# Performance work log

Hardware: AMD Instinct MI355X
Metric: run time of the kernel (lower is better)

The kernel has to match this reference:

```python
import jax, jax.numpy as jnp
import numpy as np

NEG_INF = -9e15
ALPHA = 0.2  # LeakyReLU negative slope

N = 4096
NFEAT = 512
NHID = 256
NEMBED = 128
NHEADS = 4
OUT1 = NHID // NHEADS   # 64
OUT2 = NEMBED // NHEADS # 32


def _gat_layer(x, adj_mask, W, a):
    # x: [N, F_in]; adj_mask: [N, N] bool; W: [H, F_in, F_out]; a: [H, 2*F_out]
    Fo = W.shape[-1]
    Wh = jnp.einsum('nf,hfo->hno', x, W)                     # [H, N, Fo]
    a_src = jnp.einsum('hno,ho->hn', Wh, a[:, :Fo])          # [H, N]
    a_dst = jnp.einsum('hno,ho->hn', Wh, a[:, Fo:])          # [H, N]
    e = a_src[:, :, None] + a_dst[:, None, :]                # [H, N, N]
    e = jax.nn.leaky_relu(e, negative_slope=ALPHA)
    e = jnp.where(adj_mask[None, :, :], e, NEG_INF)
    att = jax.nn.softmax(e, axis=-1)                         # [H, N, N]
    h = jnp.einsum('hnm,hmo->hno', att, Wh)                  # [H, N, Fo]
    h = jax.nn.elu(h)                                        # concat=True -> ELU
    # concat heads: [N, H*Fo]
    return jnp.transpose(h, (1, 0, 2)).reshape(x.shape[0], -1)


def setup_inputs() -> dict:
    key = jax.random.key(0)
    k1, k2, k3, k4, k5, k6 = jax.random.split(key, 6)
    x = jax.random.normal(k1, (N, NFEAT), dtype=jnp.float32)
    adj = (jax.random.uniform(k2, (N, N)) < 0.01).astype(jnp.float32)
    # per-head GAT params, xavier-uniform-like init (stacked over heads)
    def xavier(k, shape, fan):
        bound = np.sqrt(6.0 / fan)
        return jax.random.uniform(k, shape, minval=-bound, maxval=bound, dtype=jnp.float32)
    W1 = xavier(k3, (NHEADS, NFEAT, OUT1), NFEAT + OUT1)
    a1 = xavier(k4, (NHEADS, 2 * OUT1), 2 * OUT1 + 1)
    W2 = xavier(k5, (NHEADS, NHID, OUT2), NHID + OUT2)
    a2 = xavier(k6, (NHEADS, 2 * OUT2), 2 * OUT2 + 1)
    return {'x': x, 'adj': adj, 'W1': W1, 'a1': a1, 'W2': W2, 'a2': a2}


def reference(x, adj, W1, a1, W2, a2):
    # eval mode: dropout is identity
    adj_mask = adj > 0
    h1 = _gat_layer(x, adj_mask, W1, a1)    # [N, NHID]
    h2 = _gat_layer(h1, adj_mask, W2, a2)   # [N, NEMBED]
    return h2
```

## Files before the change

kernel.cpp:

```cpp
#include <hip/hip_runtime.h>
#include <hip/hip_bf16.h>
#include <cstdint>
#include <cstddef>

#define NNODES 4096
#define NHEADS 4
#define NBR_STRIDE 128

typedef __attribute__((ext_vector_type(8))) short bf16x8v;
typedef __attribute__((ext_vector_type(4))) float f32x4;

__device__ inline unsigned short bf16_rn(float f) {
    unsigned int u = __float_as_uint(f);
    u += 0x7FFFu + ((u >> 16) & 1u);
    return (unsigned short)(u >> 16);
}
__device__ inline float bf16_f32(unsigned short s) {
    return __uint_as_float(((unsigned int)s) << 16);
}

__device__ inline void build_nbr_body3(
    char* arena,
    const float* __restrict__ adj, int* __restrict__ nbr, int* __restrict__ deg,
    int row) {
    int* slots = (int*)arena;
    int* cnts  = (int*)(arena + 2048);
    int wave = threadIdx.x >> 6;
    int lane = threadIdx.x & 63;
    const float4* arow =
        reinterpret_cast<const float4*>(adj + (size_t)row * NNODES) + wave * 256;
    float4 v[4];
    #pragma unroll
    for (int it = 0; it < 4; ++it) v[it] = arow[it * 64 + lane];
    unsigned long long lt = (1ull << lane) - 1ull;
    int* slot = slots + wave * 128;
    int base = 0;
    #pragma unroll
    for (int it = 0; it < 4; ++it) {
        bool b0 = v[it].x > 0.f, b1 = v[it].y > 0.f, b2 = v[it].z > 0.f, b3 = v[it].w > 0.f;
        unsigned long long m0 = __ballot(b0);
        unsigned long long m1 = __ballot(b1);
        unsigned long long m2 = __ballot(b2);
        unsigned long long m3 = __ballot(b3);
        int pre = __popcll(m0 & lt) + __popcll(m1 & lt) +
                  __popcll(m2 & lt) + __popcll(m3 & lt);
        int pos = base + pre;
        int colb = wave * 1024 + it * 256 + lane * 4;
        if (b0) { if (pos < NBR_STRIDE) slot[pos] = colb;     pos++; }
        if (b1) { if (pos < NBR_STRIDE) slot[pos] = colb + 1; pos++; }
        if (b2) { if (pos < NBR_STRIDE) slot[pos] = colb + 2; pos++; }
        if (b3) { if (pos < NBR_STRIDE) slot[pos] = colb + 3; pos++; }
        base += __popcll(m0) + __popcll(m1) + __popcll(m2) + __popcll(m3);
    }
    if (lane == 0) cnts[wave] = base < NBR_STRIDE ? base : NBR_STRIDE;
    __syncthreads();
    int c0 = cnts[0], c1 = cnts[1], c2 = cnts[2];
    int tot = c0 + c1 + c2 + cnts[3];
    if (tot > NBR_STRIDE) tot = NBR_STRIDE;
    int t = threadIdx.x;
    if (t < tot) {
        int val;
        if (t < c0)                val = slots[t];
        else if (t < c0 + c1)      val = slots[128 + t - c0];
        else if (t < c0 + c1 + c2) val = slots[256 + t - c0 - c1];
        else                       val = slots[384 + t - c0 - c1 - c2];
        nbr[row * NBR_STRIDE + t] = val;
    }
    if (t == 0) deg[row] = tot;
}

__global__ __launch_bounds__(256) void pack_b_both_kernel(
    const float* __restrict__ W1, const float* __restrict__ W2,
    unsigned short* __restrict__ B1h, unsigned short* __restrict__ B1l,
    unsigned short* __restrict__ B2h, unsigned short* __restrict__ B2l) {
    int t = blockIdx.x * 256 + threadIdx.x;
    if (t < 256 * 512) {
        int n = t >> 9, k = t & 511;
        int h = n >> 6, o = n & 63;
        float v = W1[((size_t)h * 512 + k) * 64 + o];
        unsigned short hi = bf16_rn(v);
        B1h[t] = hi;
        B1l[t] = bf16_rn(v - bf16_f32(hi));
    } else {
        int u = t - 256 * 512;
        if (u < 128 * 256) {
            int n = u >> 8, k = u & 255;
            int h = n >> 5, o = n & 31;
            float v = W2[((size_t)h * 256 + k) * 32 + o];
            unsigned short hi = bf16_rn(v);
            B2h[u] = hi;
            B2l[u] = bf16_rn(v - bf16_f32(hi));
        }
    }
}

template <int K, int N, int FO, int BK, bool ASPLIT>
__device__ inline void gemm_body(
    char* arena,
    const float* __restrict__ A,
    const unsigned short* __restrict__ Ah, const unsigned short* __restrict__ Al,
    const unsigned short* __restrict__ Bh, const unsigned short* __restrict__ Bl,
    const float* __restrict__ a, float* __restrict__ C,
    float* __restrict__ asrc, float* __restrict__ adst,
    int bx, int by) {
    constexpr int BM = 32, BN = 64, LP = BK + 8;
    constexpr int ALD = BM * LP * 2;
    constexpr int BLD = BN * LP * 2;
    typedef unsigned short (*lds_t)[LP];
    lds_t Alh = (lds_t)(arena);
    lds_t All = (lds_t)(arena + ALD);
    lds_t Blh = (lds_t)(arena + 2 * ALD);
    lds_t Bll = (lds_t)(arena + 2 * ALD + BLD);
    float* reds = (float*)(arena + 2 * ALD + 2 * BLD);
    float* redd = (float*)(arena + 2 * ALD + 2 * BLD + 256);
    int tid = threadIdx.x;
    int wave = tid >> 6, lane = tid & 63;
    int rowBase = bx * BM;
    int colBase = by * BN;
    int wr = wave >> 1, wc = wave & 1;
    int lr = lane & 15, lk = lane >> 4;
    f32x4 acc0 = {0.f, 0.f, 0.f, 0.f};
    f32x4 acc1 = {0.f, 0.f, 0.f, 0.f};

    for (int k0 = 0; k0 < K; k0 += BK) {
        if constexpr (BK == 32) {
            int ar = tid >> 3, acf = (tid & 7) * 4;
            int br = tid >> 2, bc = (tid & 3) * 8;
            uint4 bh = *reinterpret_cast<const uint4*>(&Bh[(size_t)(colBase + br) * K + k0 + bc]);
            uint4 bl = *reinterpret_cast<const uint4*>(&Bl[(size_t)(colBase + br) * K + k0 + bc]);
            if constexpr (ASPLIT) {
                uint2 avh = *reinterpret_cast<const uint2*>(&Ah[(size_t)(rowBase + ar) * K + k0 + acf]);
                uint2 avl = *reinterpret_cast<const uint2*>(&Al[(size_t)(rowBase + ar) * K + k0 + acf]);
                __syncthreads();
                *reinterpret_cast<uint2*>(&Alh[ar][acf]) = avh;
                *reinterpret_cast<uint2*>(&All[ar][acf]) = avl;
                *reinterpret_cast<uint4*>(&Blh[br][bc]) = bh;
                *reinterpret_cast<uint4*>(&Bll[br][bc]) = bl;
            } else {
                float4 a0 = *reinterpret_cast<const float4*>(&A[(size_t)(rowBase + ar) * K + k0 + acf]);
                __syncthreads();
                ushort4 h4, l4;
                h4.x = bf16_rn(a0.x); l4.x = bf16_rn(a0.x - bf16_f32(h4.x));
                h4.y = bf16_rn(a0.y); l4.y = bf16_rn(a0.y - bf16_f32(h4.y));
                h4.z = bf16_rn(a0.z); l4.z = bf16_rn(a0.z - bf16_f32(h4.z));
                h4.w = bf16_rn(a0.w); l4.w = bf16_rn(a0.w - bf16_f32(h4.w));
                *reinterpret_cast<ushort4*>(&Alh[ar][acf]) = h4;
                *reinterpret_cast<ushort4*>(&All[ar][acf]) = l4;
                *reinterpret_cast<uint4*>(&Blh[br][bc]) = bh;
                *reinterpret_cast<uint4*>(&Bll[br][bc]) = bl;
            }
        } else {
            int ar = tid >> 3, ac = (tid & 7) * 8;
            uint4 bh0 = *reinterpret_cast<const uint4*>(&Bh[(size_t)(colBase + ar) * K + k0 + ac]);
            uint4 bl0 = *reinterpret_cast<const uint4*>(&Bl[(size_t)(colBase + ar) * K + k0 + ac]);
            uint4 bh1 = *reinterpret_cast<const uint4*>(&Bh[(size_t)(colBase + 32 + ar) * K + k0 + ac]);
            uint4 bl1 = *reinterpret_cast<const uint4*>(&Bl[(size_t)(colBase + 32 + ar) * K + k0 + ac]);
            if constexpr (ASPLIT) {
                uint4 avh = *reinterpret_cast<const uint4*>(&Ah[(size_t)(rowBase + ar) * K + k0 + ac]);
                uint4 avl = *reinterpret_cast<const uint4*>(&Al[(size_t)(rowBase + ar) * K + k0 + ac]);
                __syncthreads();
                *reinterpret_cast<uint4*>(&Alh[ar][ac]) = avh;
                *reinterpret_cast<uint4*>(&All[ar][ac]) = avl;
                *reinterpret_cast<uint4*>(&Blh[ar][ac]) = bh0;
                *reinterpret_cast<uint4*>(&Bll[ar][ac]) = bl0;
                *reinterpret_cast<uint4*>(&Blh[32 + ar][ac]) = bh1;
                *reinterpret_cast<uint4*>(&Bll[32 + ar][ac]) = bl1;
            } else {
                float4 a0 = *reinterpret_cast<const float4*>(&A[(size_t)(rowBase + ar) * K + k0 + ac]);
                float4 a1 = *reinterpret_cast<const float4*>(&A[(size_t)(rowBase + ar) * K + k0 + ac + 4]);
                __syncthreads();
                ushort4 h4, l4;
                h4.x = bf16_rn(a0.x); l4.x = bf16_rn(a0.x - bf16_f32(h4.x));
                h4.y = bf16_rn(a0.y); l4.y = bf16_rn(a0.y - bf16_f32(h4.y));
                h4.z = bf16_rn(a0.z); l4.z = bf16_rn(a0.z - bf16_f32(h4.z));
                h4.w = bf16_rn(a0.w); l4.w = bf16_rn(a0.w - bf16_f32(h4.w));
                *reinterpret_cast<ushort4*>(&Alh[ar][ac]) = h4;
                *reinterpret_cast<ushort4*>(&All[ar][ac]) = l4;
                h4.x = bf16_rn(a1.x); l4.x = bf16_rn(a1.x - bf16_f32(h4.x));
                h4.y = bf16_rn(a1.y); l4.y = bf16_rn(a1.y - bf16_f32(h4.y));
                h4.z = bf16_rn(a1.z); l4.z = bf16_rn(a1.z - bf16_f32(h4.z));
                h4.w = bf16_rn(a1.w); l4.w = bf16_rn(a1.w - bf16_f32(h4.w));
                *reinterpret_cast<ushort4*>(&Alh[ar][ac + 4]) = h4;
                *reinterpret_cast<ushort4*>(&All[ar][ac + 4]) = l4;
                *reinterpret_cast<uint4*>(&Blh[ar][ac]) = bh0;
                *reinterpret_cast<uint4*>(&Bll[ar][ac]) = bl0;
                *reinterpret_cast<uint4*>(&Blh[32 + ar][ac]) = bh1;
                *reinterpret_cast<uint4*>(&Bll[32 + ar][ac]) = bl1;
            }
        }
        __syncthreads();
        #pragma unroll
        for (int ks = 0; ks < BK / 32; ++ks) {
            int kb = ks * 32 + lk * 8;
            bf16x8v ah = *reinterpret_cast<const bf16x8v*>(&Alh[wr * 16 + lr][kb]);
            bf16x8v al = *reinterpret_cast<const bf16x8v*>(&All[wr * 16 + lr][kb]);
            bf16x8v b0h = *reinterpret_cast<const bf16x8v*>(&Blh[wc * 32 + lr][kb]);
            bf16x8v b0l = *reinterpret_cast<const bf16x8v*>(&Bll[wc * 32 + lr][kb]);
            bf16x8v b1h = *reinterpret_cast<const bf16x8v*>(&Blh[wc * 32 + 16 + lr][kb]);
            bf16x8v b1l = *reinterpret_cast<const bf16x8v*>(&Bll[wc * 32 + 16 + lr][kb]);
            acc0 = __builtin_amdgcn_mfma_f32_16x16x32_bf16(ah, b0h, acc0, 0, 0, 0);
            acc0 = __builtin_amdgcn_mfma_f32_16x16x32_bf16(ah, b0l, acc0, 0, 0, 0);
            acc0 = __builtin_amdgcn_mfma_f32_16x16x32_bf16(al, b0h, acc0, 0, 0, 0);
            acc1 = __builtin_amdgcn_mfma_f32_16x16x32_bf16(ah, b1h, acc1, 0, 0, 0);
            acc1 = __builtin_amdgcn_mfma_f32_16x16x32_bf16(ah, b1l, acc1, 0, 0, 0);
            acc1 = __builtin_amdgcn_mfma_f32_16x16x32_bf16(al, b1h, acc1, 0, 0, 0);
        }
    }
    int crow = rowBase + wr * 16 + lk * 4;
    int ccol = colBase + wc * 32 + lr;
    #pragma unroll
    for (int r = 0; r < 4; ++r) {
        C[(size_t)(crow + r) * N + ccol]      = acc0[r];
        C[(size_t)(crow + r) * N + ccol + 16] = acc1[r];
    }
    int n0 = colBase + wc * 32 + lr;
    int hh = n0 / FO;
    int o0 = n0 % FO;
    int o1 = o0 + 16;
    const float* av = a + hh * 2 * FO;
    float aS0 = av[o0], aS1 = av[o1];
    float aD0 = av[FO + o0], aD1 = av[FO + o1];
    float sv[4], dv[4];
    #pragma unroll
    for (int r = 0; r < 4; ++r) {
        sv[r] = acc0[r] * aS0 + acc1[r] * aS1;
        dv[r] = acc0[r] * aD0 + acc1[r] * aD1;
        #pragma unroll
        for (int msk = 1; msk < 16; msk <<= 1) {
            sv[r] += __shfl_xor(sv[r], msk);
            dv[r] += __shfl_xor(dv[r], msk);
        }
    }
    if constexpr (FO == 64) {
        if (lr == 0) {
            #pragma unroll
            for (int r = 0; r < 4; ++r) {
                reds[wc * 32 + wr * 16 + lk * 4 + r] = sv[r];
                redd[wc * 32 + wr * 16 + lk * 4 + r] = dv[r];
            }
        }
        __syncthreads();
        if (tid < BM) {
            int row = tid;
            asrc[(size_t)(rowBase + row) * NHEADS + by] = reds[row] + reds[32 + row];
            adst[(size_t)(rowBase + row) * NHEADS + by] = redd[row] + redd[32 + row];
        }
    } else {
        if (lr == 0) {
            #pragma unroll
            for (int r = 0; r < 4; ++r) {
                int row = rowBase + wr * 16 + lk * 4 + r;
                asrc[(size_t)row * NHEADS + hh] = sv[r];
                adst[(size_t)row * NHEADS + hh] = dv[r];
            }
        }
    }
}

__global__ __launch_bounds__(256) void fused1_kernel(
    const float* __restrict__ adj, int* __restrict__ nbr, int* __restrict__ deg,
    const float* __restrict__ x,
    const unsigned short* __restrict__ B1h, const unsigned short* __restrict__ B1l,
    const float* __restrict__ a1, float* __restrict__ Wh1,
    float* __restrict__ as1, float* __restrict__ ad1) {
    __shared__ __align__(16) char arena[15872];
    int b = blockIdx.x;
    if (b < 512) {
        gemm_body<512, 256, 64, 32, false>(arena, x, nullptr, nullptr,
                                           B1h, B1l, a1, Wh1, as1, ad1,
                                           b & 127, b >> 7);
    } else {
        build_nbr_body3(arena, adj, nbr, deg, b - 512);
    }
}

__global__ __launch_bounds__(256) void gemm2_kernel(
    const unsigned short* __restrict__ Ah, const unsigned short* __restrict__ Al,
    const unsigned short* __restrict__ Bh, const unsigned short* __restrict__ Bl,
    const float* __restrict__ a, float* __restrict__ C,
    float* __restrict__ asrc, float* __restrict__ adst) {
    __shared__ __align__(16) char arena[28160];
    gemm_body<256, 128, 32, 64, true>(arena, nullptr, Ah, Al, Bh, Bl,
                                      a, C, asrc, adst, blockIdx.x, blockIdx.y);
}

template <int FO, bool SPLITOUT>
__global__ __launch_bounds__(256) void agg_kernel(
    const float* __restrict__ Wh,
    const float* __restrict__ asrc, const float* __restrict__ adst,
    const int* __restrict__ nbr, const int* __restrict__ deg,
    float* __restrict__ out,
    unsigned short* __restrict__ outh, unsigned short* __restrict__ outl) {
    int wslot = threadIdx.x >> 6;
    int lane = threadIdx.x & 63;
    int n = blockIdx.x;
    int h = wslot;
    int dg = deg[n];
    const int* lst = nbr + n * NBR_STRIDE;
    float my_as = asrc[(size_t)n * NHEADS + h];

    constexpr int STRIDE = NHEADS * FO;
    constexpr int LPR = FO / 4;
    constexpr int NPS = 64 / LPR;
    int sub = lane / LPR;
    int dim4 = (lane % LPR) * 4;
    const float* whp = Wh + h * FO + dim4;

    float m = -1e30f, s = 0.f;
    f32x4 acc = {0.f, 0.f, 0.f, 0.f};

    int k = sub;
    for (; k + NPS < dg; k += 2 * NPS) {
        int cA = lst[k];
        int cB = lst[k + NPS];
        float eA = my_as + adst[(size_t)cA * NHEADS + h];
        float eB = my_as + adst[(size_t)cB * NHEADS + h];
        eA = eA >= 0.f ? eA : 0.2f * eA;
        eB = eB >= 0.f ? eB : 0.2f * eB;
        float4 vA = *reinterpret_cast<const float4*>(&whp[(size_t)cA * STRIDE]);
        float4 vB = *reinterpret_cast<const float4*>(&whp[(size_t)cB * STRIDE]);
        float mn = fmaxf(m, fmaxf(eA, eB));
        float sc = __expf(m - mn);
        float pA = __expf(eA - mn);
        float pB = __expf(eB - mn);
        s = s * sc + pA + pB;
        acc[0] = acc[0] * sc + pA * vA.x + pB * vB.x;
        acc[1] = acc[1] * sc + pA * vA.y + pB * vB.y;
        acc[2] = acc[2] * sc + pA * vA.z + pB * vB.z;
        acc[3] = acc[3] * sc + pA * vA.w + pB * vB.w;
        m = mn;
    }
    if (k < dg) {
        int c = lst[k];
        float e = my_as + adst[(size_t)c * NHEADS + h];
        e = e >= 0.f ? e : 0.2f * e;
        float4 v = *reinterpret_cast<const float4*>(&whp[(size_t)c * STRIDE]);
        float mn = fmaxf(m, e);
        float sc = __expf(m - mn);
        float p = __expf(e - mn);
        s = s * sc + p;
        acc[0] = acc[0] * sc + p * v.x;
        acc[1] = acc[1] * sc + p * v.y;
        acc[2] = acc[2] * sc + p * v.z;
        acc[3] = acc[3] * sc + p * v.w;
        m = mn;
    }
    #pragma unroll
    for (int off = LPR; off < 64; off <<= 1) {
        float m2 = __shfl_xor(m, off);
        float s2 = __shfl_xor(s, off);
        float a0 = __shfl_xor(acc[0], off);
        float a1 = __shfl_xor(acc[1], off);
        float a2 = __shfl_xor(acc[2], off);
        float a3 = __shfl_xor(acc[3], off);
        float mn = fmaxf(m, m2);
        float sa = __expf(m - mn);
        float sb = __expf(m2 - mn);
        s = s * sa + s2 * sb;
        acc[0] = acc[0] * sa + a0 * sb;
        acc[1] = acc[1] * sa + a1 * sb;
        acc[2] = acc[2] * sa + a2 * sb;
        acc[3] = acc[3] * sa + a3 * sb;
        m = mn;
    }
    if (lane < LPR) {
        float inv = 1.0f / s;
        float r0 = acc[0] * inv;
        float r1 = acc[1] * inv;
        float r2 = acc[2] * inv;
        float r3 = acc[3] * inv;
        r0 = r0 > 0.f ? r0 : expm1f(r0);
        r1 = r1 > 0.f ? r1 : expm1f(r1);
        r2 = r2 > 0.f ? r2 : expm1f(r2);
        r3 = r3 > 0.f ? r3 : expm1f(r3);
        size_t idx = (size_t)n * STRIDE + h * FO + dim4;
        if constexpr (SPLITOUT) {
            ushort4 hv, lv;
            hv.x = bf16_rn(r0); lv.x = bf16_rn(r0 - bf16_f32(hv.x));
            hv.y = bf16_rn(r1); lv.y = bf16_rn(r1 - bf16_f32(hv.y));
            hv.z = bf16_rn(r2); lv.z = bf16_rn(r2 - bf16_f32(hv.z));
            hv.w = bf16_rn(r3); lv.w = bf16_rn(r3 - bf16_f32(hv.w));
            *reinterpret_cast<ushort4*>(&outh[idx]) = hv;
            *reinterpret_cast<ushort4*>(&outl[idx]) = lv;
        } else {
            *reinterpret_cast<float4*>(&out[idx]) = make_float4(r0, r1, r2, r3);
        }
    }
}

extern "C" void kernel_launch(void* const* d_in, const int* in_sizes, int n_in,
                              void* d_out, int out_size, void* d_ws, size_t ws_size,
                              hipStream_t stream) {
    const float* x   = (const float*)d_in[0];
    const float* adj = (const float*)d_in[1];
    const float* W1  = (const float*)d_in[2];
    const float* a1  = (const float*)d_in[3];
    const float* W2  = (const float*)d_in[4];
    const float* a2  = (const float*)d_in[5];
    float* outp = (float*)d_out;

    char* p = (char*)d_ws;
    auto alloc = [&](size_t bytes) -> void* {
        void* r = (void*)p;
        p += (bytes + 255) & ~(size_t)255;
        return r;
    };
    int*   nbr = (int*)alloc((size_t)NNODES * NBR_STRIDE * 4);
    int*   deg = (int*)alloc((size_t)NNODES * 4);
    unsigned short* B1h = (unsigned short*)alloc((size_t)256 * 512 * 2);
    unsigned short* B1l = (unsigned short*)alloc((size_t)256 * 512 * 2);
    unsigned short* B2h = (unsigned short*)alloc((size_t)128 * 256 * 2);
    unsigned short* B2l = (unsigned short*)alloc((size_t)128 * 256 * 2);
    float* Wh1 = (float*)alloc((size_t)NNODES * 256 * 4);
    float* as1 = (float*)alloc((size_t)NHEADS * NNODES * 4);
    float* ad1 = (float*)alloc((size_t)NHEADS * NNODES * 4);
    unsigned short* h1h = (unsigned short*)alloc((size_t)NNODES * 256 * 2);
    unsigned short* h1l = (unsigned short*)alloc((size_t)NNODES * 256 * 2);
    float* Wh2 = (float*)alloc((size_t)NNODES * 128 * 4);
    float* as2 = (float*)alloc((size_t)NHEADS * NNODES * 4);
    float* ad2 = (float*)alloc((size_t)NHEADS * NNODES * 4);

    pack_b_both_kernel<<<dim3((256 * 512 + 128 * 256) / 256), dim3(256), 0, stream>>>(
        W1, W2, B1h, B1l, B2h, B2l);
    fused1_kernel<<<dim3(512 + NNODES), dim3(256), 0, stream>>>(
        adj, nbr, deg, x, B1h, B1l, a1, Wh1, as1, ad1);
    agg_kernel<64, true><<<dim3(NNODES), dim3(256), 0, stream>>>(
        Wh1, as1, ad1, nbr, deg, nullptr, h1h, h1l);
    gemm2_kernel<<<dim3(NNODES / 32, 2), dim3(256), 0, stream>>>(
        h1h, h1l, B2h, B2l, a2, Wh2, as2, ad2);
    agg_kernel<32, false><<<dim3(NNODES), dim3(256), 0, stream>>>(
        Wh2, as2, ad2, nbr, deg, outp, nullptr, nullptr);
}
```

Before: 65.17 us.

## Fuse all GAT stages into one cooperative persistent kernel with grid syncs

Replaces the five separate launches (weight pack, GEMM1 plus neighbor build, agg1, GEMM2, agg2) with a single cooperative kernel of 2048 blocks that uses grid.sync between stages. Each block loops over several rows for the neighbor build and handles two nodes per aggregation phase. GEMM2 now runs with a smaller tile config on 256 blocks. The aim is to remove kernel launch gaps and tail effects. The cost is grid-wide barriers and reduced parallelism per stage, with a fallback to the old launches if the cooperative launch is unavailable or occupancy is too low.

```diff
diff --git a/kernel.cpp b/kernel.cpp
--- a/kernel.cpp
+++ b/kernel.cpp
@@ -1,11 +1,15 @@
 #include <hip/hip_runtime.h>
 #include <hip/hip_bf16.h>
+#include <hip/hip_cooperative_groups.h>
 #include <cstdint>
 #include <cstddef>
+
+namespace cg = cooperative_groups;
 
 #define NNODES 4096
 #define NHEADS 4
 #define NBR_STRIDE 128
+#define NBLK 2048
 
 typedef __attribute__((ext_vector_type(8))) short bf16x8v;
 typedef __attribute__((ext_vector_type(4))) float f32x4;
@@ -67,13 +71,14 @@
         nbr[row * NBR_STRIDE + t] = val;
     }
     if (t == 0) deg[row] = tot;
-}
-
-__global__ __launch_bounds__(256) void pack_b_both_kernel(
+    __syncthreads();
+}
+
+__device__ inline void pack_body(
     const float* __restrict__ W1, const float* __restrict__ W2,
     unsigned short* __restrict__ B1h, unsigned short* __restrict__ B1l,
-    unsigned short* __restrict__ B2h, unsigned short* __restrict__ B2l) {
-    int t = blockIdx.x * 256 + threadIdx.x;
+    unsigned short* __restrict__ B2h, unsigned short* __restrict__ B2l,
+    int t) {
     if (t < 256 * 512) {
         int n = t >> 9, k = t & 511;
         int h = n >> 6, o = n & 63;
@@ -245,6 +250,7 @@
             asrc[(size_t)(rowBase + row) * NHEADS + by] = reds[row] + reds[32 + row];
             adst[(size_t)(rowBase + row) * NHEADS + by] = redd[row] + redd[32 + row];
         }
+        __syncthreads();
     } else {
         if (lr == 0) {
             #pragma unroll
@@ -257,43 +263,16 @@
     }
 }
 
-__global__ __launch_bounds__(256) void fused1_kernel(
-    const float* __restrict__ adj, int* __restrict__ nbr, int* __restrict__ deg,
-    const float* __restrict__ x,
-    const unsigned short* __restrict__ B1h, const unsigned short* __restrict__ B1l,
-    const float* __restrict__ a1, float* __restrict__ Wh1,
-    float* __restrict__ as1, float* __restrict__ ad1) {
-    __shared__ __align__(16) char arena[15872];
-    int b = blockIdx.x;
-    if (b < 512) {
-        gemm_body<512, 256, 64, 32, false>(arena, x, nullptr, nullptr,
-                                           B1h, B1l, a1, Wh1, as1, ad1,
-                                           b & 127, b >> 7);
-    } else {
-        build_nbr_body3(arena, adj, nbr, deg, b - 512);
-    }
-}
-
-__global__ __launch_bounds__(256) void gemm2_kernel(
-    const unsigned short* __restrict__ Ah, const unsigned short* __restrict__ Al,
-    const unsigned short* __restrict__ Bh, const unsigned short* __restrict__ Bl,
-    const float* __restrict__ a, float* __restrict__ C,
-    float* __restrict__ asrc, float* __restrict__ adst) {
-    __shared__ __align__(16) char arena[28160];
-    gemm_body<256, 128, 32, 64, true>(arena, nullptr, Ah, Al, Bh, Bl,
-                                      a, C, asrc, adst, blockIdx.x, blockIdx.y);
-}
-
 template <int FO, bool SPLITOUT>
-__global__ __launch_bounds__(256) void agg_kernel(
+__device__ inline void agg_body(
     const float* __restrict__ Wh,
     const float* __restrict__ asrc, const float* __restrict__ adst,
     const int* __restrict__ nbr, const int* __restrict__ deg,
     float* __restrict__ out,
-    unsigned short* __restrict__ outh, unsigned short* __restrict__ outl) {
+    unsigned short* __restrict__ outh, unsigned short* __restrict__ outl,
+    int n) {
     int wslot = threadIdx.x >> 6;
     int lane = threadIdx.x & 63;
-    int n = blockIdx.x;
     int h = wslot;
     int dg = deg[n];
     const int* lst = nbr + n * NBR_STRIDE;
@@ -388,6 +367,101 @@
     }
 }
 
+__global__ __launch_bounds__(256, 8) void mega_kernel(
+    const float* __restrict__ adj, const float* __restrict__ x,
+    const float* __restrict__ W1, const float* __restrict__ a1,
+    const float* __restrict__ W2, const float* __restrict__ a2,
+    int* __restrict__ nbr, int* __restrict__ deg,
+    unsigned short* __restrict__ B1h, unsigned short* __restrict__ B1l,
+    unsigned short* __restrict__ B2h, unsigned short* __restrict__ B2l,
+    float* __restrict__ Wh1, float* __restrict__ as1, float* __restrict__ ad1,
+    unsigned short* __restrict__ h1h, unsigned short* __restrict__ h1l,
+    float* __restrict__ Wh2, float* __restrict__ as2, float* __restrict__ ad2,
+    float* __restrict__ out) {
+    __shared__ __align__(16) char arena[15872];
+    cg::grid_group grid = cg::this_grid();
+    int b = blockIdx.x;
+
+    {
+        int t = b * 256 + (int)threadIdx.x;
+        if (t < 256 * 512 + 128 * 256)
+            pack_body(W1, W2, B1h, B1l, B2h, B2l, t);
+    }
+    grid.sync();
+
+    if (b < 512) {
+        gemm_body<512, 256, 64, 32, false>(arena, x, nullptr, nullptr,
+                                           B1h, B1l, a1, Wh1, as1, ad1,
+                                           b & 127, b >> 7);
+    } else {
+        int nb = b - 512;
+        #pragma unroll
+        for (int i = 0; i < 3; ++i) {
+            int row = nb + 1536 * i;
+            if (row < NNODES) build_nbr_body3(arena, adj, nbr, deg, row);
+        }
+    }
+    grid.sync();
+
+    agg_body<64, true>(Wh1, as1, ad1, nbr, deg, nullptr, h1h, h1l, b * 2);
+    agg_body<64, true>(Wh1, as1, ad1, nbr, deg, nullptr, h1h, h1l, b * 2 + 1);
+    grid.sync();
+
+    if (b < 256) {
+        gemm_body<256, 128, 32, 32, true>(arena, nullptr, h1h, h1l,
+                                          B2h, B2l, a2, Wh2, as2, ad2,
+                                          b & 127, b >> 7);
+    }
+    grid.sync();
+
+    agg_body<32, false>(Wh2, as2, ad2, nbr, deg, out, nullptr, nullptr, b * 2);
+    agg_body<32, false>(Wh2, as2, ad2, nbr, deg, out, nullptr, nullptr, b * 2 + 1);
+}
+
+__global__ __launch_bounds__(256) void pack_b_both_kernel(
+    const float* __restrict__ W1, const float* __restrict__ W2,
+    unsigned short* __restrict__ B1h, unsigned short* __restrict__ B1l,
+    unsigned short* __restrict__ B2h, unsigned short* __restrict__ B2l) {
+    pack_body(W1, W2, B1h, B1l, B2h, B2l, blockIdx.x * 256 + threadIdx.x);
+}
+
+__global__ __launch_bounds__(256) void fused1_kernel(
+    const float* __restrict__ adj, int* __restrict__ nbr, int* __restrict__ deg,
+    const float* __restrict__ x,
+    const unsigned short* __restrict__ B1h, const unsigned short* __restrict__ B1l,
+    const float* __restrict__ a1, float* __restrict__ Wh1,
+    float* __restrict__ as1, float* __restrict__ ad1) {
+    __shared__ __align__(16) char arena[15872];
+    int b = blockIdx.x;
+    if (b < 512) {
+        gemm_body<512, 256, 64, 32, false>(arena, x, nullptr, nullptr,
+                                           B1h, B1l, a1, Wh1, as1, ad1,
+                                           b & 127, b >> 7);
+    } else {
+        build_nbr_body3(arena, adj, nbr, deg, b - 512);
+    }
+}
+
+__global__ __launch_bounds__(256) void gemm2_kernel(
+    const unsigned short* __restrict__ Ah, const unsigned short* __restrict__ Al,
+    const unsigned short* __restrict__ Bh, const unsigned short* __restrict__ Bl,
+    const float* __restrict__ a, float* __restrict__ C,
+    float* __restrict__ asrc, float* __restrict__ adst) {
+    __shared__ __align__(16) char arena[28160];
+    gemm_body<256, 128, 32, 64, true>(arena, nullptr, Ah, Al, Bh, Bl,
+                                      a, C, asrc, adst, blockIdx.x, blockIdx.y);
+}
+
+template <int FO, bool SPLITOUT>
+__global__ __launch_bounds__(256) void agg_kernel(
+    const float* __restrict__ Wh,
+    const float* __restrict__ asrc, const float* __restrict__ adst,
+    const int* __restrict__ nbr, const int* __restrict__ deg,
+    float* __restrict__ out,
+    unsigned short* __restrict__ outh, unsigned short* __restrict__ outl) {
+    agg_body<FO, SPLITOUT>(Wh, asrc, adst, nbr, deg, out, outh, outl, blockIdx.x);
+}
+
 extern "C" void kernel_launch(void* const* d_in, const int* in_sizes, int n_in,
                               void* d_out, int out_size, void* d_ws, size_t ws_size,
                               hipStream_t stream) {
@@ -420,6 +494,25 @@
     float* as2 = (float*)alloc((size_t)NHEADS * NNODES * 4);
     float* ad2 = (float*)alloc((size_t)NHEADS * NNODES * 4);
 
+    int blocksPerCU = 0;
+    hipError_t qe = hipOccupancyMaxActiveBlocksPerMultiprocessor(
+        &blocksPerCU, (const void*)mega_kernel, 256, 0);
+    bool coop = (qe == hipSuccess) && (blocksPerCU * 256 >= NBLK);
+
+    if (coop) {
+        void* args[] = {
+            (void*)&adj, (void*)&x, (void*)&W1, (void*)&a1, (void*)&W2, (void*)&a2,
+            (void*)&nbr, (void*)&deg, (void*)&B1h, (void*)&B1l, (void*)&B2h, (void*)&B2l,
+            (void*)&Wh1, (void*)&as1, (void*)&ad1, (void*)&h1h, (void*)&h1l,
+            (void*)&Wh2, (void*)&as2, (void*)&ad2, (void*)&outp
+        };
+        hipError_t le = hipLaunchCooperativeKernel((const void*)mega_kernel,
+                                                   dim3(NBLK), dim3(256),
+                                                   args, 0, stream);
+        if (le == hipSuccess) return;
+        (void)hipGetLastError();
+    }
+
     pack_b_both_kernel<<<dim3((256 * 512 + 128 * 256) / 256), dim3(256), 0, stream>>>(
         W1, W2, B1h, B1l, B2h, B2l);
     fused1_kernel<<<dim3(512 + NNODES), dim3(256), 0, stream>>>(
```

Result: no change. 64.67 us (-0.8%).
